# Kernel tuning notes

Hardware: AMD Instinct MI355X
Metric: run time of the kernel (lower is better)

Reference implementation:

```python
import jax, jax.numpy as jnp
import numpy as np

N_NODES = 50000
N_EDGES = 800000
IN_DIM = 128
ADD = 8
HIDDEN = 256
OUT_DIM = 128


def gcn_conv(x, src, dst, W, b, n_nodes):
    """PyG GCNConv: linear -> sym-normalized scatter-add with self-loops -> bias."""
    loop = jnp.arange(n_nodes, dtype=src.dtype)
    s = jnp.concatenate([src, loop])
    d = jnp.concatenate([dst, loop])
    deg = jax.ops.segment_sum(jnp.ones(s.shape[0], dtype=x.dtype), d, num_segments=n_nodes)
    dinv = jnp.where(deg > 0, jax.lax.rsqrt(deg), 0.0)
    norm = dinv[s] * dinv[d]                       # [E+N]
    h = x @ W                                      # [N, F_out]
    msg = h[s] * norm[:, None]                     # [E+N, F_out]
    out = jax.ops.segment_sum(msg, d, num_segments=n_nodes)
    return out + b


def prelu(x, a):
    return jnp.where(x >= 0, x, a * x)


def setup_inputs() -> dict:
    key = jax.random.key(0)
    ks = jax.random.split(key, 8)
    x = jax.random.normal(ks[0], (N_NODES, IN_DIM), dtype=jnp.float32)
    edge_index = jax.random.randint(ks[1], (2, N_EDGES), 0, N_NODES, dtype=jnp.int64)
    id_vec = jax.random.normal(ks[2], (ADD,), dtype=jnp.float32)
    # Glorot-ish init for linear weights, PReLU slope 0.25 (torch default)
    W1 = jax.random.normal(ks[3], (IN_DIM + ADD, HIDDEN), dtype=jnp.float32) * 0.05
    b1 = jnp.zeros((HIDDEN,), dtype=jnp.float32)
    a1 = jnp.full((HIDDEN,), 0.25, dtype=jnp.float32)
    W2 = jax.random.normal(ks[4], (HIDDEN, OUT_DIM), dtype=jnp.float32) * 0.05
    b2 = jnp.zeros((OUT_DIM,), dtype=jnp.float32)
    a2 = jnp.full((OUT_DIM,), 0.25, dtype=jnp.float32)
    return {"x": x, "edge_index": edge_index, "id": id_vec,
            "W1": W1, "b1": b1, "a1": a1, "W2": W2, "b2": b2, "a2": a2}


def reference(x, edge_index, id, W1, b1, a1, W2, b2, a2):
    n = x.shape[0]
    src, dst = edge_index[0], edge_index[1]
    # tile id vector onto every node and concat along features
    xi = jnp.concatenate([x, jnp.broadcast_to(id[None, :], (n, id.shape[0]))], axis=1)
    h = gcn_conv(xi, src, dst, W1, b1, n)
    h = prelu(h, a1)
    h = gcn_conv(h, src, dst, W2, b2, n)
    h = prelu(h, a2)
    return h
```

## Files before the change

kernel.cpp:

```cpp
#include <hip/hip_runtime.h>


constexpr int NN = 50000;
constexpr int NE = 800000;
constexpr int NBUCK = 196;
constexpr int TILE = 2048;
constexpr int NSCAT = (NE + TILE - 1) / TILE;

typedef __attribute__((ext_vector_type(8))) short short8;
typedef __attribute__((ext_vector_type(4))) float floatx4;

__device__ inline void bsplit(float v, unsigned short& hi, unsigned short& lo) {
  unsigned u = __float_as_uint(v);
  hi = (unsigned short)(u >> 16);
  float rem = v - __uint_as_float(u & 0xffff0000u);
  lo = (unsigned short)(__float_as_uint(rem) >> 16);
}

__device__ inline unsigned short bf16_rtne(float v) {
  unsigned u = __float_as_uint(v);
  return (unsigned short)((u + 0x7fffu + ((u >> 16) & 1u)) >> 16);
}

__device__ inline float bflo(unsigned u) { return __uint_as_float(u << 16); }
__device__ inline float bfhi(unsigned u) { return __uint_as_float(u & 0xffff0000u); }


__global__ __launch_bounds__(256) void tile_count_kernel(const int* __restrict__ ei,
                                                         int* __restrict__ tilecnt) {
  __shared__ int h[NBUCK];
  int t = threadIdx.x;
  for (int i = t; i < NBUCK; i += 256) h[i] = 0;
  __syncthreads();
  int base = blockIdx.x * TILE;
  int end = base + TILE; if (end > NE) end = NE;
  for (int e = base + t; e < end; e += 256) atomicAdd(&h[ei[NE + e] >> 8], 1);
  __syncthreads();
  for (int i = t; i < NBUCK; i += 256) tilecnt[blockIdx.x * NBUCK + i] = h[i];
}

__global__ void tile_scan_kernel(const int* __restrict__ tilecnt, int* __restrict__ tpre,
                                 int* __restrict__ bbase, int* __restrict__ bcnt) {
  __shared__ int sums[256];
  int b = threadIdx.x;
  int run = 0;
  if (b < NBUCK) {
    for (int ti = 0; ti < NSCAT; ++ti) {
      int idx = ti * NBUCK + b;
      int v = tilecnt[idx];
      tpre[idx] = run;
      run += v;
    }
  }
  sums[b] = (b < NBUCK) ? run : 0;
  __syncthreads();
  for (int off = 1; off < 256; off <<= 1) {
    int u = (b >= off) ? sums[b - off] : 0;
    __syncthreads();
    sums[b] += u;
    __syncthreads();
  }
  if (b < NBUCK) {
    bbase[b] = sums[b] - run;
    bcnt[b] = run;
  }
}

__global__ __launch_bounds__(256) void bucket_scatter_kernel(
    const int* __restrict__ ei, const int* __restrict__ tilecnt,
    const int* __restrict__ tpre, const int* __restrict__ bbase,
    unsigned* __restrict__ ebuf) {
  __shared__ int lbase[NBUCK], gb[NBUCK], lcur[NBUCK], ssc[256];
  __shared__ unsigned stage[TILE];
  int t = threadIdx.x;
  int tile = blockIdx.x;
  int base = tile * TILE;
  int cntTile = NE - base; if (cntTile > TILE) cntTile = TILE;
  int h = (t < NBUCK) ? tilecnt[tile * NBUCK + t] : 0;
  ssc[t] = h;
  __syncthreads();
  for (int off = 1; off < 256; off <<= 1) {
    int u = (t >= off) ? ssc[t - off] : 0;
    __syncthreads();
    ssc[t] += u;
    __syncthreads();
  }
  if (t < NBUCK) {
    int ex = ssc[t] - h;
    lbase[t] = ex;
    lcur[t] = ex;
    gb[t] = bbase[t] + tpre[tile * NBUCK + t];
  }
  __syncthreads();
  for (int e = base + t; e < base + cntTile; e += 256) {
    int s = ei[e];
    int d = ei[NE + e];
    int b = d >> 8;
    int pos = atomicAdd(&lcur[b], 1);
    stage[pos] = ((unsigned)(d & 255) << 16) | (unsigned)s;
  }
  __syncthreads();
  for (int i = t; i < cntTile; i += 256) {
    int lo = 0, hi = NBUCK - 1;
    while (lo < hi) {
      int mid = (lo + hi + 1) >> 1;
      if (lbase[mid] <= i) lo = mid; else hi = mid - 1;
    }
    ebuf[gb[lo] + (i - lbase[lo])] = stage[i];
  }
}

__global__ __launch_bounds__(256) void bucket_csr_kernel(
    const unsigned* __restrict__ ebuf, const int* __restrict__ bbase,
    const int* __restrict__ bcnt, int* __restrict__ offs, int* __restrict__ col,
    float* __restrict__ dinv) {
  __shared__ int cnt[256], cur[256], sums[256];
  int b = blockIdx.x, t = threadIdx.x;
  int node0 = b << 8;
  cnt[t] = 0;
  __syncthreads();
  int g0 = bbase[b], g1 = g0 + bcnt[b];
  for (int i = g0 + t; i < g1; i += 256) atomicAdd(&cnt[ebuf[i] >> 16], 1);
  __syncthreads();
  int c = cnt[t];
  sums[t] = c;
  __syncthreads();
  for (int off = 1; off < 256; off <<= 1) {
    int u = (t >= off) ? sums[t - off] : 0;
    __syncthreads();
    sums[t] += u;
    __syncthreads();
  }
  int ex = sums[t] - c;
  cur[t] = ex;
  int node = node0 + t;
  if (node < NN) {
    offs[node] = g0 + ex;
    dinv[node] = rsqrtf((float)(c + 1));
  }
  __syncthreads();
  for (int i = g0 + t; i < g1; i += 256) {
    unsigned v = ebuf[i];
    int pos = atomicAdd(&cur[v >> 16], 1);
    col[g0 + pos] = (int)(v & 0xffffu);
  }
  if (b == 0 && t == 0) offs[NN] = NE;
}

__global__ void svec_kernel(const float* __restrict__ dinv, const int* __restrict__ offs,
                            const int* __restrict__ col, float* __restrict__ Svec) {
  int d = blockIdx.x * blockDim.x + threadIdx.x;
  if (d >= NN) return;
  float s = 0.f;
  int end = offs[d + 1];
  for (int p = offs[d]; p < end; ++p) s += dinv[col[p]];
  float dd = dinv[d];
  Svec[d] = dd * (dd + s);
}

__global__ void cvec_kernel(const float* __restrict__ idv, const float* __restrict__ W1,
                            float* __restrict__ cvec) {
  int m = threadIdx.x;
  float c = 0.f;
#pragma unroll
  for (int j = 0; j < 8; ++j) c += idv[j] * W1[(128 + j) * 256 + m];
  cvec[m] = c;
}

__global__ void scale_x_kernel(const float* __restrict__ x, const float* __restrict__ dinv,
                               unsigned short* __restrict__ xsb) {
  int i = blockIdx.x * blockDim.x + threadIdx.x;
  if (i < NN * 32) {
    float dd = dinv[i >> 5];
    float4 v = ((const float4*)x)[i];
    ushort4 o;
    o.x = bf16_rtne(v.x * dd);
    o.y = bf16_rtne(v.y * dd);
    o.z = bf16_rtne(v.z * dd);
    o.w = bf16_rtne(v.w * dd);
    ((ushort4*)xsb)[i] = o;
  }
}

template <int K, int N>
__global__ void pack_b_kernel(const float* __restrict__ W, unsigned short* __restrict__ Bhi,
                              unsigned short* __restrict__ Blo) {
  int id = blockIdx.x * 256 + threadIdx.x;
  if (id >= K * N) return;
  constexpr int KC = K / 32;
  int j = id & 7;
  int lane = (id >> 3) & 63;
  int rest = id >> 9;
  int c = rest % KC;
  int nt = rest / KC;
  int k = c * 32 + (lane >> 4) * 8 + j;
  int n = nt * 16 + (lane & 15);
  unsigned short hi, lo;
  bsplit(W[(size_t)k * N + n], hi, lo);
  Bhi[id] = hi;
  Blo[id] = lo;
}

template <int MODE>
__global__ __launch_bounds__(256) void agg_kernel(
    const unsigned short* __restrict__ in, const float* __restrict__ dinv,
    const int* __restrict__ offs, const int* __restrict__ col,
    const float* __restrict__ bias, const float* __restrict__ alpha,
    unsigned short* __restrict__ outhi, unsigned short* __restrict__ outlo,
    float* __restrict__ outf) {
  const uint2* inb = (const uint2*)in;
  int t = threadIdx.x;
  int node = blockIdx.x * 4 + (t >> 6);
  int lane = t & 63;
  int r = lane & 31;
  int half = lane >> 5;
  int beg = offs[node], end = offs[node + 1];

  float4 a0 = make_float4(0.f, 0.f, 0.f, 0.f);
  float4 a1 = make_float4(0.f, 0.f, 0.f, 0.f);
  int p = beg + half;
  for (; p + 6 < end; p += 8) {
    int s0 = col[p];
    int s1 = col[p + 2];
    int s2 = col[p + 4];
    int s3 = col[p + 6];
    uint2 v0 = inb[(size_t)s0 * 32 + r];
    uint2 v1 = inb[(size_t)s1 * 32 + r];
    uint2 v2 = inb[(size_t)s2 * 32 + r];
    uint2 v3 = inb[(size_t)s3 * 32 + r];
    a0.x += bflo(v0.x); a0.y += bfhi(v0.x); a0.z += bflo(v0.y); a0.w += bfhi(v0.y);
    a1.x += bflo(v1.x); a1.y += bfhi(v1.x); a1.z += bflo(v1.y); a1.w += bfhi(v1.y);
    a0.x += bflo(v2.x); a0.y += bfhi(v2.x); a0.z += bflo(v2.y); a0.w += bfhi(v2.y);
    a1.x += bflo(v3.x); a1.y += bfhi(v3.x); a1.z += bflo(v3.y); a1.w += bfhi(v3.y);
  }
  for (; p < end; p += 2) {
    uint2 v0 = inb[(size_t)col[p] * 32 + r];
    a0.x += bflo(v0.x); a0.y += bfhi(v0.x); a0.z += bflo(v0.y); a0.w += bfhi(v0.y);
  }
  float4 acc = make_float4(a0.x + a1.x, a0.y + a1.y, a0.z + a1.z, a0.w + a1.w);
  acc.x += __shfl_xor(acc.x, 32);
  acc.y += __shfl_xor(acc.y, 32);
  acc.z += __shfl_xor(acc.z, 32);
  acc.w += __shfl_xor(acc.w, 32);

  float dd = dinv[node];
  if (half == 0) {
    uint2 sv = inb[(size_t)node * 32 + r];
    acc.x = dd * (acc.x + bflo(sv.x));
    acc.y = dd * (acc.y + bfhi(sv.x));
    acc.z = dd * (acc.z + bflo(sv.y));
    acc.w = dd * (acc.w + bfhi(sv.y));
    if (MODE == 0) {
      ushort4 h4, l4;
      bsplit(acc.x, h4.x, l4.x);
      bsplit(acc.y, h4.y, l4.y);
      bsplit(acc.z, h4.z, l4.z);
      bsplit(acc.w, h4.w, l4.w);
      ((ushort4*)outhi)[(size_t)node * 32 + r] = h4;
      ((ushort4*)outlo)[(size_t)node * 32 + r] = l4;
    } else {
      float4 b = ((const float4*)bias)[r];
      float4 al = ((const float4*)alpha)[r];
      acc.x += b.x; acc.y += b.y; acc.z += b.z; acc.w += b.w;
      acc.x = (acc.x >= 0.f) ? acc.x : al.x * acc.x;
      acc.y = (acc.y >= 0.f) ? acc.y : al.y * acc.y;
      acc.z = (acc.z >= 0.f) ? acc.z : al.z * acc.z;
      acc.w = (acc.w >= 0.f) ? acc.w : al.w * acc.w;
      ((float4*)outf)[(size_t)node * 32 + r] = acc;
    }
  }
}

template <int K, int N, int MODE>
__global__ __launch_bounds__(256) void gemm_mfma_kernel(
    const unsigned short* __restrict__ Ahi, const unsigned short* __restrict__ Alo,
    const unsigned short* __restrict__ Bhi, const unsigned short* __restrict__ Blo,
    const float* __restrict__ Svec, const float* __restrict__ cvec,
    const float* __restrict__ bias, const float* __restrict__ alpha,
    const float* __restrict__ rowscale,
    unsigned short* __restrict__ Chi, unsigned short* __restrict__ Clo,
    unsigned short* __restrict__ Cb) {
  constexpr int KC = K / 32;
  constexpr int NT = N / 16;
  int wave = threadIdx.x >> 6;
  int lane = threadIdx.x & 63;
  int row0 = blockIdx.x * 64 + wave * 16;
  if (row0 >= NN) return;
  int m = lane & 15, quad = lane >> 4;
  int arow = row0 + m;

  short8 ah[KC], al[KC];
  const unsigned short* ap = Ahi + (size_t)arow * K + quad * 8;
  const unsigned short* alp = Alo + (size_t)arow * K + quad * 8;
#pragma unroll
  for (int c = 0; c < KC; ++c) {
    ah[c] = *(const short8*)(ap + c * 32);
    al[c] = *(const short8*)(alp + c * 32);
  }

  float sv[4];
#pragma unroll
  for (int i = 0; i < 4; ++i) {
    int r = row0 + quad * 4 + i;
    sv[i] = (MODE == 1) ? Svec[r] : rowscale[r];
  }

#pragma unroll 1
  for (int nt = 0; nt < NT; ++nt) {
    floatx4 acc = {0.f, 0.f, 0.f, 0.f};
#pragma unroll
    for (int c = 0; c < KC; ++c) {
      short8 bh = *(const short8*)(Bhi + ((size_t)(nt * KC + c) * 64 + lane) * 8);
      short8 bl = *(const short8*)(Blo + ((size_t)(nt * KC + c) * 64 + lane) * 8);
      acc = __builtin_amdgcn_mfma_f32_16x16x32_bf16(ah[c], bh, acc, 0, 0, 0);
      acc = __builtin_amdgcn_mfma_f32_16x16x32_bf16(ah[c], bl, acc, 0, 0, 0);
      acc = __builtin_amdgcn_mfma_f32_16x16x32_bf16(al[c], bh, acc, 0, 0, 0);
    }
    int c0 = nt * 16 + m;
    if (MODE == 1) {
      float cv = cvec[c0], bb = bias[c0], aa = alpha[c0];
#pragma unroll
      for (int i = 0; i < 4; ++i) {
        int r = row0 + quad * 4 + i;
        float v = acc[i] + sv[i] * cv + bb;
        v = (v >= 0.f) ? v : aa * v;
        unsigned short hi, lo;
        bsplit(v, hi, lo);
        Chi[(size_t)r * N + c0] = hi;
        Clo[(size_t)r * N + c0] = lo;
      }
    } else {
#pragma unroll
      for (int i = 0; i < 4; ++i) {
        int r = row0 + quad * 4 + i;
        Cb[(size_t)r * N + c0] = bf16_rtne(acc[i] * sv[i]);
      }
    }
  }
}

extern "C" void kernel_launch(void* const* d_in, const int* in_sizes, int n_in,
                              void* d_out, int out_size, void* d_ws, size_t ws_size,
                              hipStream_t stream) {
  const float* x = (const float*)d_in[0];
  const int* ei = (const int*)d_in[1];
  const float* idv = (const float*)d_in[2];
  const float* W1 = (const float*)d_in[3];
  const float* b1 = (const float*)d_in[4];
  const float* a1 = (const float*)d_in[5];
  const float* W2 = (const float*)d_in[6];
  const float* b2 = (const float*)d_in[7];
  const float* a2 = (const float*)d_in[8];
  float* out = (float*)d_out;

  char* w = (char*)d_ws;
  size_t off = 0;
  auto alloc = [&](size_t bytes) -> void* {
    void* p = w + off;
    off += bytes;
    off = (off + 255) & ~(size_t)255;
    return p;
  };
  int* tilecnt = (int*)alloc((size_t)NSCAT * NBUCK * 4);
  int* tpre = (int*)alloc((size_t)NSCAT * NBUCK * 4);
  int* bbase = (int*)alloc((size_t)NBUCK * 4);
  int* bcnt = (int*)alloc((size_t)NBUCK * 4);
  unsigned* ebuf = (unsigned*)alloc((size_t)NE * 4);
  float* dinv = (float*)alloc((size_t)NN * 4);
  float* Svec = (float*)alloc((size_t)NN * 4);
  int* offs = (int*)alloc((size_t)(NN + 1) * 4);
  int* col = (int*)alloc((size_t)NE * 4);
  float* cvec = (float*)alloc(256 * 4);
  unsigned short* xsb = (unsigned short*)alloc((size_t)NN * 128 * 2);
  unsigned short* aggxhi = (unsigned short*)alloc((size_t)NN * 128 * 2);
  unsigned short* aggxlo = (unsigned short*)alloc((size_t)NN * 128 * 2);
  unsigned short* h1hi = (unsigned short*)alloc((size_t)NN * 256 * 2);
  unsigned short* h1lo = (unsigned short*)alloc((size_t)NN * 256 * 2);
  unsigned short* h2b = (unsigned short*)alloc((size_t)NN * 128 * 2);
  unsigned short* B1hi = (unsigned short*)alloc(128 * 256 * 2);
  unsigned short* B1lo = (unsigned short*)alloc(128 * 256 * 2);
  unsigned short* B2hi = (unsigned short*)alloc(256 * 128 * 2);
  unsigned short* B2lo = (unsigned short*)alloc(256 * 128 * 2);

  tile_count_kernel<<<NSCAT, 256, 0, stream>>>(ei, tilecnt);
  tile_scan_kernel<<<1, 256, 0, stream>>>(tilecnt, tpre, bbase, bcnt);
  bucket_scatter_kernel<<<NSCAT, 256, 0, stream>>>(ei, tilecnt, tpre, bbase, ebuf);
  bucket_csr_kernel<<<NBUCK, 256, 0, stream>>>(ebuf, bbase, bcnt, offs, col, dinv);

  svec_kernel<<<(NN + 255) / 256, 256, 0, stream>>>(dinv, offs, col, Svec);
  cvec_kernel<<<1, 256, 0, stream>>>(idv, W1, cvec);
  scale_x_kernel<<<(NN * 32 + 255) / 256, 256, 0, stream>>>(x, dinv, xsb);
  pack_b_kernel<128, 256><<<(128 * 256 + 255) / 256, 256, 0, stream>>>(W1, B1hi, B1lo);
  pack_b_kernel<256, 128><<<(256 * 128 + 255) / 256, 256, 0, stream>>>(W2, B2hi, B2lo);

  agg_kernel<0><<<NN / 4, 256, 0, stream>>>(xsb, dinv, offs, col, nullptr, nullptr,
                                            aggxhi, aggxlo, nullptr);

  gemm_mfma_kernel<128, 256, 1><<<(NN + 63) / 64, 256, 0, stream>>>(
      aggxhi, aggxlo, B1hi, B1lo, Svec, cvec, b1, a1, nullptr, h1hi, h1lo, nullptr);

  gemm_mfma_kernel<256, 128, 2><<<(NN + 63) / 64, 256, 0, stream>>>(
      h1hi, h1lo, B2hi, B2lo, nullptr, nullptr, nullptr, nullptr, dinv,
      nullptr, nullptr, h2b);

  agg_kernel<1><<<NN / 4, 256, 0, stream>>>(h2b, dinv, offs, col, b2, a2,
                                            nullptr, nullptr, out);
}
```

Baseline: 300.7 us.

## Parallelize tile scan, merge small prep kernels, deepen aggregation unroll

The old single-block serial tile scan, where each of 196 threads walked 391 tiles, becomes one block per bucket doing a parallel prefix scan, plus a small kernel for the bucket bases. The svec, cvec, scale_x and two pack kernels are merged into two launches to cut launch overhead. The aggregation gather loop is unrolled to 8 loads per iteration with 4 accumulators to raise memory-level parallelism. The risks are higher register pressure in agg_kernel and one extra launch for the bucket bases.

```diff
diff --git a/kernel.cpp b/kernel.cpp
--- a/kernel.cpp
+++ b/kernel.cpp
@@ -39,31 +39,42 @@
   for (int i = t; i < NBUCK; i += 256) tilecnt[blockIdx.x * NBUCK + i] = h[i];
 }
 
-__global__ void tile_scan_kernel(const int* __restrict__ tilecnt, int* __restrict__ tpre,
-                                 int* __restrict__ bbase, int* __restrict__ bcnt) {
-  __shared__ int sums[256];
-  int b = threadIdx.x;
-  int run = 0;
-  if (b < NBUCK) {
-    for (int ti = 0; ti < NSCAT; ++ti) {
-      int idx = ti * NBUCK + b;
-      int v = tilecnt[idx];
-      tpre[idx] = run;
-      run += v;
-    }
-  }
-  sums[b] = (b < NBUCK) ? run : 0;
+__global__ __launch_bounds__(256) void tile_scan_a_kernel(const int* __restrict__ tilecnt,
+                                                          int* __restrict__ tpre,
+                                                          int* __restrict__ bcnt) {
+  __shared__ int sm[256];
+  int b = blockIdx.x, t = threadIdx.x;
+  int i0 = 2 * t, i1 = 2 * t + 1;
+  int v0 = (i0 < NSCAT) ? tilecnt[i0 * NBUCK + b] : 0;
+  int v1 = (i1 < NSCAT) ? tilecnt[i1 * NBUCK + b] : 0;
+  int s = v0 + v1;
+  sm[t] = s;
   __syncthreads();
   for (int off = 1; off < 256; off <<= 1) {
-    int u = (b >= off) ? sums[b - off] : 0;
-    __syncthreads();
-    sums[b] += u;
-    __syncthreads();
-  }
-  if (b < NBUCK) {
-    bbase[b] = sums[b] - run;
-    bcnt[b] = run;
-  }
+    int u = (t >= off) ? sm[t - off] : 0;
+    __syncthreads();
+    sm[t] += u;
+    __syncthreads();
+  }
+  int ex = sm[t] - s;
+  if (i0 < NSCAT) tpre[i0 * NBUCK + b] = ex;
+  if (i1 < NSCAT) tpre[i1 * NBUCK + b] = ex + v0;
+  if (t == 255) bcnt[b] = sm[255];
+}
+
+__global__ void bucket_base_kernel(const int* __restrict__ bcnt, int* __restrict__ bbase) {
+  __shared__ int sm[256];
+  int t = threadIdx.x;
+  int v = (t < NBUCK) ? bcnt[t] : 0;
+  sm[t] = v;
+  __syncthreads();
+  for (int off = 1; off < 256; off <<= 1) {
+    int u = (t >= off) ? sm[t - off] : 0;
+    __syncthreads();
+    sm[t] += u;
+    __syncthreads();
+  }
+  if (t < NBUCK) bbase[t] = sm[t] - v;
 }
 
 __global__ __launch_bounds__(256) void bucket_scatter_kernel(
@@ -147,46 +158,35 @@
   if (b == 0 && t == 0) offs[NN] = NE;
 }
 
-__global__ void svec_kernel(const float* __restrict__ dinv, const int* __restrict__ offs,
-                            const int* __restrict__ col, float* __restrict__ Svec) {
-  int d = blockIdx.x * blockDim.x + threadIdx.x;
-  if (d >= NN) return;
-  float s = 0.f;
-  int end = offs[d + 1];
-  for (int p = offs[d]; p < end; ++p) s += dinv[col[p]];
-  float dd = dinv[d];
-  Svec[d] = dd * (dd + s);
-}
-
-__global__ void cvec_kernel(const float* __restrict__ idv, const float* __restrict__ W1,
-                            float* __restrict__ cvec) {
-  int m = threadIdx.x;
-  float c = 0.f;
-#pragma unroll
-  for (int j = 0; j < 8; ++j) c += idv[j] * W1[(128 + j) * 256 + m];
-  cvec[m] = c;
-}
-
-__global__ void scale_x_kernel(const float* __restrict__ x, const float* __restrict__ dinv,
-                               unsigned short* __restrict__ xsb) {
-  int i = blockIdx.x * blockDim.x + threadIdx.x;
-  if (i < NN * 32) {
-    float dd = dinv[i >> 5];
-    float4 v = ((const float4*)x)[i];
+__global__ __launch_bounds__(256) void post_csr_kernel(
+    const float* __restrict__ x, const float* __restrict__ dinv,
+    const int* __restrict__ offs, const int* __restrict__ col,
+    unsigned short* __restrict__ xsb, float* __restrict__ Svec) {
+  int id = blockIdx.x * 256 + threadIdx.x;
+  if (id < NN * 32) {
+    float dd = dinv[id >> 5];
+    float4 v = ((const float4*)x)[id];
     ushort4 o;
     o.x = bf16_rtne(v.x * dd);
     o.y = bf16_rtne(v.y * dd);
     o.z = bf16_rtne(v.z * dd);
     o.w = bf16_rtne(v.w * dd);
-    ((ushort4*)xsb)[i] = o;
+    ((ushort4*)xsb)[id] = o;
+  } else {
+    int d = id - NN * 32;
+    if (d < NN) {
+      float s = 0.f;
+      int end = offs[d + 1];
+      for (int p = offs[d]; p < end; ++p) s += dinv[col[p]];
+      float dd = dinv[d];
+      Svec[d] = dd * (dd + s);
+    }
   }
 }
 
 template <int K, int N>
-__global__ void pack_b_kernel(const float* __restrict__ W, unsigned short* __restrict__ Bhi,
-                              unsigned short* __restrict__ Blo) {
-  int id = blockIdx.x * 256 + threadIdx.x;
-  if (id >= K * N) return;
+__device__ inline void pack_one(const float* __restrict__ W, unsigned short* __restrict__ Bhi,
+                                unsigned short* __restrict__ Blo, int id) {
   constexpr int KC = K / 32;
   int j = id & 7;
   int lane = (id >> 3) & 63;
@@ -199,6 +199,25 @@
   bsplit(W[(size_t)k * N + n], hi, lo);
   Bhi[id] = hi;
   Blo[id] = lo;
+}
+
+__global__ void prep_weights_kernel(const float* __restrict__ W1, const float* __restrict__ W2,
+                                    const float* __restrict__ idv,
+                                    unsigned short* __restrict__ B1hi, unsigned short* __restrict__ B1lo,
+                                    unsigned short* __restrict__ B2hi, unsigned short* __restrict__ B2lo,
+                                    float* __restrict__ cvec) {
+  int id = blockIdx.x * 256 + threadIdx.x;
+  if (id < 32768) {
+    pack_one<128, 256>(W1, B1hi, B1lo, id);
+  } else if (id < 65536) {
+    pack_one<256, 128>(W2, B2hi, B2lo, id - 32768);
+  } else if (id < 65536 + 256) {
+    int m = id - 65536;
+    float c = 0.f;
+#pragma unroll
+    for (int j = 0; j < 8; ++j) c += idv[j] * W1[(128 + j) * 256 + m];
+    cvec[m] = c;
+  }
 }
 
 template <int MODE>
@@ -218,26 +237,45 @@
 
   float4 a0 = make_float4(0.f, 0.f, 0.f, 0.f);
   float4 a1 = make_float4(0.f, 0.f, 0.f, 0.f);
+  float4 a2 = make_float4(0.f, 0.f, 0.f, 0.f);
+  float4 a3 = make_float4(0.f, 0.f, 0.f, 0.f);
   int p = beg + half;
-  for (; p + 6 < end; p += 8) {
-    int s0 = col[p];
-    int s1 = col[p + 2];
-    int s2 = col[p + 4];
-    int s3 = col[p + 6];
+  for (; p + 14 < end; p += 16) {
+    int s0 = col[p];      int s1 = col[p + 2];
+    int s2 = col[p + 4];  int s3 = col[p + 6];
+    int s4 = col[p + 8];  int s5 = col[p + 10];
+    int s6 = col[p + 12]; int s7 = col[p + 14];
     uint2 v0 = inb[(size_t)s0 * 32 + r];
     uint2 v1 = inb[(size_t)s1 * 32 + r];
     uint2 v2 = inb[(size_t)s2 * 32 + r];
     uint2 v3 = inb[(size_t)s3 * 32 + r];
+    uint2 v4 = inb[(size_t)s4 * 32 + r];
+    uint2 v5 = inb[(size_t)s5 * 32 + r];
+    uint2 v6 = inb[(size_t)s6 * 32 + r];
+    uint2 v7 = inb[(size_t)s7 * 32 + r];
     a0.x += bflo(v0.x); a0.y += bfhi(v0.x); a0.z += bflo(v0.y); a0.w += bfhi(v0.y);
     a1.x += bflo(v1.x); a1.y += bfhi(v1.x); a1.z += bflo(v1.y); a1.w += bfhi(v1.y);
-    a0.x += bflo(v2.x); a0.y += bfhi(v2.x); a0.z += bflo(v2.y); a0.w += bfhi(v2.y);
-    a1.x += bflo(v3.x); a1.y += bfhi(v3.x); a1.z += bflo(v3.y); a1.w += bfhi(v3.y);
-  }
-  for (; p < end; p += 2) {
+    a2.x += bflo(v2.x); a2.y += bfhi(v2.x); a2.z += bflo(v2.y); a2.w += bfhi(v2.y);
+    a3.x += bflo(v3.x); a3.y += bfhi(v3.x); a3.z += bflo(v3.y); a3.w += bfhi(v3.y);
+    a0.x += bflo(v4.x); a0.y += bfhi(v4.x); a0.z += bflo(v4.y); a0.w += bfhi(v4.y);
+    a1.x += bflo(v5.x); a1.y += bfhi(v5.x); a1.z += bflo(v5.y); a1.w += bfhi(v5.y);
+    a2.x += bflo(v6.x); a2.y += bfhi(v6.x); a2.z += bflo(v6.y); a2.w += bfhi(v6.y);
+    a3.x += bflo(v7.x); a3.y += bfhi(v7.x); a3.z += bflo(v7.y); a3.w += bfhi(v7.y);
+  }
+  for (; p + 2 < end; p += 4) {
+    int s0 = col[p];
+    int s1 = col[p + 2];
+    uint2 v0 = inb[(size_t)s0 * 32 + r];
+    uint2 v1 = inb[(size_t)s1 * 32 + r];
+    a0.x += bflo(v0.x); a0.y += bfhi(v0.x); a0.z += bflo(v0.y); a0.w += bfhi(v0.y);
+    a1.x += bflo(v1.x); a1.y += bfhi(v1.x); a1.z += bflo(v1.y); a1.w += bfhi(v1.y);
+  }
+  if (p < end) {
     uint2 v0 = inb[(size_t)col[p] * 32 + r];
     a0.x += bflo(v0.x); a0.y += bfhi(v0.x); a0.z += bflo(v0.y); a0.w += bfhi(v0.y);
   }
-  float4 acc = make_float4(a0.x + a1.x, a0.y + a1.y, a0.z + a1.z, a0.w + a1.w);
+  float4 acc = make_float4((a0.x + a1.x) + (a2.x + a3.x), (a0.y + a1.y) + (a2.y + a3.y),
+                           (a0.z + a1.z) + (a2.z + a3.z), (a0.w + a1.w) + (a2.w + a3.w));
   acc.x += __shfl_xor(acc.x, 32);
   acc.y += __shfl_xor(acc.y, 32);
   acc.z += __shfl_xor(acc.z, 32);
@@ -383,15 +421,15 @@
   unsigned short* B2lo = (unsigned short*)alloc(256 * 128 * 2);
 
   tile_count_kernel<<<NSCAT, 256, 0, stream>>>(ei, tilecnt);
-  tile_scan_kernel<<<1, 256, 0, stream>>>(tilecnt, tpre, bbase, bcnt);
+  tile_scan_a_kernel<<<NBUCK, 256, 0, stream>>>(tilecnt, tpre, bcnt);
+  bucket_base_kernel<<<1, 256, 0, stream>>>(bcnt, bbase);
   bucket_scatter_kernel<<<NSCAT, 256, 0, stream>>>(ei, tilecnt, tpre, bbase, ebuf);
   bucket_csr_kernel<<<NBUCK, 256, 0, stream>>>(ebuf, bbase, bcnt, offs, col, dinv);
 
-  svec_kernel<<<(NN + 255) / 256, 256, 0, stream>>>(dinv, offs, col, Svec);
-  cvec_kernel<<<1, 256, 0, stream>>>(idv, W1, cvec);
-  scale_x_kernel<<<(NN * 32 + 255) / 256, 256, 0, stream>>>(x, dinv, xsb);
-  pack_b_kernel<128, 256><<<(128 * 256 + 255) / 256, 256, 0, stream>>>(W1, B1hi, B1lo);
-  pack_b_kernel<256, 128><<<(256 * 128 + 255) / 256, 256, 0, stream>>>(W2, B2hi, B2lo);
+  prep_weights_kernel<<<(65536 + 256 + 255) / 256, 256, 0, stream>>>(
+      W1, W2, idv, B1hi, B1lo, B2hi, B2lo, cvec);
+  post_csr_kernel<<<(NN * 32 + NN + 255) / 256, 256, 0, stream>>>(
+      x, dinv, offs, col, xsb, Svec);
 
   agg_kernel<0><<<NN / 4, 256, 0, stream>>>(xsb, dinv, offs, col, nullptr, nullptr,
                                             aggxhi, aggxlo, nullptr);
```

After: 272.3 us. -9.4%, faster.
